# Performance work log

Measured on AMD Instinct MI355X. Metric: run time of the kernel, lower is better.

## Reference

```python
import jax, jax.numpy as jnp
import numpy as np

WS = 16      # window_size
FW = 1       # focal_window -> 3x3 grid of focal windows
FF = 2       # focal_factor (avg-pool for non-center windows)
NH = 8       # num_heads

_OFFSETS = [(di, dj) for di in range(-FW, FW + 1) for dj in range(-FW, FW + 1)]
# tokens contributed by each focal window (center keeps full res, neighbors pooled)
_COUNTS = np.array([WS * WS if (di == 0 and dj == 0) else (WS // FF) ** 2 for di, dj in _OFFSETS])
# center window gets zero bias, peripheral windows get -position_bias (intent of add_focal_bias)
_MULTS = np.array([0.0 if (di == 0 and dj == 0) else -1.0 for di, dj in _OFFSETS], dtype=np.float32)


def _gather_focal(x):
    """x: (B,H,W,C) -> (B*nW, kv_len, C) focal key/value tokens per window."""
    B, H, W, C = x.shape
    nH, nWg = H // WS, W // WS
    xp = jnp.pad(x, ((0, 0), (WS, WS), (WS, WS), (0, 0)), mode='reflect')
    # padded window grid: (B, nH+2, nWg+2, WS, WS, C)
    g = xp.reshape(B, nH + 2, WS, nWg + 2, WS, C).transpose(0, 1, 3, 2, 4, 5)
    parts = []
    for di, dj in _OFFSETS:
        w = g[:, 1 + di:1 + di + nH, 1 + dj:1 + dj + nWg]  # (B,nH,nWg,WS,WS,C)
        if di == 0 and dj == 0:
            t = w.reshape(B, nH, nWg, WS * WS, C)
        else:
            p = WS // FF  # avg_pool2d(kernel=stride=FF)
            t = w.reshape(B, nH, nWg, p, FF, p, FF, C).mean(axis=(4, 6)).reshape(B, nH, nWg, p * p, C)
        parts.append(t)
    kv = jnp.concatenate(parts, axis=3)  # (B,nH,nWg,kv_len,C)
    return kv.reshape(B * nH * nWg, -1, C)


def _bias_tokens(position_bias):
    # (NH, 9) -> (NH, kv_len): per-focal-window bias broadcast over its tokens
    scaled = position_bias * jnp.asarray(_MULTS)[None, :]
    return jnp.repeat(scaled, _COUNTS, axis=1)


def reference(x, Wq, bq, Wk, bk, Wv, bv, Wo, bo, position_bias):
    B, H, W, C = x.shape
    hd = C // NH
    scale = hd ** -0.5
    nH, nWg = H // WS, W // WS
    # window partition: (B*nW, WS*WS, C)
    xw = x.reshape(B, nH, WS, nWg, WS, C).transpose(0, 1, 3, 2, 4, 5).reshape(-1, WS * WS, C)
    kv = _gather_focal(x)  # (B*nW, kv_len, C)
    q = (xw @ Wq + bq).reshape(-1, WS * WS, NH, hd).transpose(0, 2, 1, 3)
    k = (kv @ Wk + bk).reshape(kv.shape[0], -1, NH, hd).transpose(0, 2, 1, 3)
    v = (kv @ Wv + bv).reshape(kv.shape[0], -1, NH, hd).transpose(0, 2, 1, 3)
    attn = jnp.einsum('whqd,whkd->whqk', q, k) * scale
    attn = attn + _bias_tokens(position_bias)[None, :, None, :]
    attn = jax.nn.softmax(attn, axis=-1)
    out = jnp.einsum('whqk,whkd->whqd', attn, v).transpose(0, 2, 1, 3).reshape(-1, WS * WS, C)
    out = out @ Wo + bo
    # window reverse
    out = out.reshape(B, nH, nWg, WS, WS, C).transpose(0, 1, 3, 2, 4, 5).reshape(B, H, W, C)
    return out


def setup_inputs() -> dict:
    key = jax.random.key(0)
    ks = jax.random.split(key, 10)
    D = 384
    w = lambda k: jax.random.normal(k, (D, D), dtype=jnp.float32) * 0.02
    b = lambda k: jax.random.normal(k, (D,), dtype=jnp.float32) * 0.02
    return {
        'x': jax.random.normal(ks[0], (2, 128, 128, D), dtype=jnp.float32),
        'Wq': w(ks[1]), 'bq': b(ks[2]),
        'Wk': w(ks[3]), 'bk': b(ks[4]),
        'Wv': w(ks[5]), 'bv': b(ks[6]),
        'Wo': w(ks[7]), 'bo': b(ks[8]),
        'position_bias': jax.random.normal(ks[9], (NH, 9), dtype=jnp.float32) * 0.02,
    }
```

## Files before the change

kernel.cpp:

```cpp
#include <hip/hip_runtime.h>
#include <hip/hip_bf16.h>

#define NTOK 32768
#define LOG2E 1.4426950408889634f

typedef __attribute__((ext_vector_type(8))) short bf16x8;
typedef __attribute__((ext_vector_type(4))) float f32x4;

__device__ __forceinline__ float bf2f(unsigned short u) {
  return __uint_as_float(((unsigned int)u) << 16);
}
__device__ __forceinline__ unsigned short f2bf(float f) {
  union { __hip_bfloat16 h; unsigned short u; } cv;
  cv.h = __float2bfloat16(f);
  return cv.u;
}
__device__ __forceinline__ float fast_exp2(float x) {
#if __has_builtin(__builtin_amdgcn_exp2f)
  return __builtin_amdgcn_exp2f(x);
#else
  return exp2f(x);
#endif
}

__device__ __forceinline__ void gload16(const void* g, void* l) {
  __builtin_amdgcn_global_load_lds(
      (const __attribute__((address_space(1))) unsigned int*)(unsigned long long)g,
      (__attribute__((address_space(3))) unsigned int*)(unsigned long long)l, 16, 0, 0);
}

__global__ __launch_bounds__(256) void convert_x(const float* __restrict__ x,
                                                 unsigned short* __restrict__ xb) {
  const int i = (blockIdx.x * 256 + threadIdx.x) * 8;
  float4 a = *(const float4*)(x + i);
  float4 b = *(const float4*)(x + i + 4);
  *(ushort4*)(xb + i)     = make_ushort4(f2bf(a.x), f2bf(a.y), f2bf(a.z), f2bf(a.w));
  *(ushort4*)(xb + i + 4) = make_ushort4(f2bf(b.x), f2bf(b.y), f2bf(b.z), f2bf(b.w));
}

__global__ __launch_bounds__(256) void transpose_w(const float* __restrict__ Wq,
                                                   const float* __restrict__ Wk,
                                                   const float* __restrict__ Wv,
                                                   const float* __restrict__ Wo,
                                                   unsigned short* __restrict__ Wt) {
  __shared__ float tile[32][33];
  const int wsel = blockIdx.z;
  const float* W = (wsel == 0) ? Wq : (wsel == 1) ? Wk : (wsel == 2) ? Wv : Wo;
  unsigned short* out = Wt + (size_t)wsel * 147456;
  const int k0 = blockIdx.x * 32, n0 = blockIdx.y * 32;
  const int r = threadIdx.x >> 3, c4 = (threadIdx.x & 7) * 4;
  float4 v = *(const float4*)&W[(size_t)(k0 + r) * 384 + n0 + c4];
  tile[r][c4 + 0] = v.x; tile[r][c4 + 1] = v.y; tile[r][c4 + 2] = v.z; tile[r][c4 + 3] = v.w;
  __syncthreads();
  ushort4 o = make_ushort4(f2bf(tile[c4 + 0][r]), f2bf(tile[c4 + 1][r]),
                           f2bf(tile[c4 + 2][r]), f2bf(tile[c4 + 3][r]));
  *(ushort4*)&out[(size_t)(n0 + r) * 384 + k0 + c4] = o;
}

__global__ __launch_bounds__(128) void pool_kernel(const unsigned short* __restrict__ xb,
                                                   unsigned short* __restrict__ P) {
  int blk = blockIdx.x;
  int b = blk / 6400;
  int rem = blk - b * 6400;
  int p0 = rem / 80, p1 = rem - p0 * 80;
  int i0 = 2 * p0 - 16, i1 = i0 + 1;
  int j0 = 2 * p1 - 16, j1 = j0 + 1;
  int r0 = i0 < 0 ? -i0 : (i0 > 127 ? 254 - i0 : i0);
  int r1 = i1 < 0 ? -i1 : (i1 > 127 ? 254 - i1 : i1);
  int c0 = j0 < 0 ? -j0 : (j0 > 127 ? 254 - j0 : j0);
  int c1 = j1 < 0 ? -j1 : (j1 > 127 ? 254 - j1 : j1);
  const unsigned short* s00 = xb + (((size_t)b * 128 + r0) * 128 + c0) * 384;
  const unsigned short* s01 = xb + (((size_t)b * 128 + r0) * 128 + c1) * 384;
  const unsigned short* s10 = xb + (((size_t)b * 128 + r1) * 128 + c0) * 384;
  const unsigned short* s11 = xb + (((size_t)b * 128 + r1) * 128 + c1) * 384;
  unsigned short* dst = P + (size_t)blk * 384;
  for (int c = threadIdx.x; c < 384; c += 128)
    dst[c] = f2bf(0.25f * (bf2f(s00[c]) + bf2f(s01[c]) + bf2f(s10[c]) + bf2f(s11[c])));
}

__global__ __launch_bounds__(256) void mfma_proj_fused(
    const unsigned short* __restrict__ xb, const unsigned short* __restrict__ P,
    const unsigned short* __restrict__ Wt,
    const float* __restrict__ bq, const float* __restrict__ bk, const float* __restrict__ bv,
    unsigned short* __restrict__ Qb, unsigned short* __restrict__ Kcat,
    unsigned short* __restrict__ Vcat) {
  const int xx = blockIdx.x, yy = blockIdx.y;
  const unsigned short* X;
  int wsel; size_t off;
  if (xx < 9) { X = xb; wsel = xx / 3; off = 0; }
  else { if (yy >= 100) return; X = P; wsel = 1 + (xx - 9) / 3; off = (size_t)NTOK * 384; }
  const float* bias = (wsel == 0) ? bq : (wsel == 1) ? bk : bv;
  unsigned short* Y = ((wsel == 0) ? Qb : (wsel == 1) ? Kcat : Vcat) + off;
  const unsigned short* Wm = Wt + (size_t)wsel * 147456;
  const int n0 = ((xx < 9) ? (xx % 3) : ((xx - 9) % 3)) * 128;
  const int m0 = yy * 128;

  __shared__ __attribute__((aligned(16))) unsigned short As[128 * 32];
  __shared__ __attribute__((aligned(16))) unsigned short Bs[128 * 32];
  const int t = threadIdx.x;
  const int w = t >> 6, l = t & 63, l15 = l & 15, g = l >> 4;
  const int wm = w >> 1, wn = w & 1;

  f32x4 acc[4][4];
  #pragma unroll
  for (int i = 0; i < 4; ++i)
    #pragma unroll
    for (int j = 0; j < 4; ++j) acc[i][j] = {0.f, 0.f, 0.f, 0.f};

  for (int k0 = 0; k0 < 384; k0 += 32) {
    __syncthreads();
    #pragma unroll
    for (int a = 0; a < 2; ++a) {
      const int c = w * 2 + a;
      const int row = c * 16 + (l >> 2), kc = (l & 3) * 8;
      gload16(X  + (size_t)(m0 + row) * 384 + k0 + kc, As + c * 512);
      gload16(Wm + (size_t)(n0 + row) * 384 + k0 + kc, Bs + c * 512);
    }
    __syncthreads();
    bf16x8 af[4], bfr[4];
    #pragma unroll
    for (int mi = 0; mi < 4; ++mi)
      af[mi] = *(const bf16x8*)(As + (wm * 64 + mi * 16 + l15) * 32 + g * 8);
    #pragma unroll
    for (int nj = 0; nj < 4; ++nj)
      bfr[nj] = *(const bf16x8*)(Bs + (wn * 64 + nj * 16 + l15) * 32 + g * 8);
    #pragma unroll
    for (int mi = 0; mi < 4; ++mi)
      #pragma unroll
      for (int nj = 0; nj < 4; ++nj)
        acc[mi][nj] = __builtin_amdgcn_mfma_f32_16x16x32_bf16(af[mi], bfr[nj], acc[mi][nj], 0, 0, 0);
  }

  float bv4[4];
  #pragma unroll
  for (int nj = 0; nj < 4; ++nj) bv4[nj] = bias[n0 + wn * 64 + nj * 16 + l15];
  #pragma unroll
  for (int mi = 0; mi < 4; ++mi)
    #pragma unroll
    for (int nj = 0; nj < 4; ++nj)
      #pragma unroll
      for (int r = 0; r < 4; ++r) {
        const size_t row = m0 + wm * 64 + mi * 16 + g * 4 + r;
        const size_t col = n0 + wn * 64 + nj * 16 + l15;
        Y[row * 384 + col] = f2bf(acc[mi][nj][r] + bv4[nj]);
      }
}

__global__ __launch_bounds__(256) void mfma_proj_out(const unsigned short* __restrict__ X,
                                                     const unsigned short* __restrict__ Wm,
                                                     const float* __restrict__ bias,
                                                     float* __restrict__ Y) {
  const int n0 = blockIdx.x * 128, m0 = blockIdx.y * 128;
  __shared__ __attribute__((aligned(16))) unsigned short As[128 * 32];
  __shared__ __attribute__((aligned(16))) unsigned short Bs[128 * 32];
  const int t = threadIdx.x;
  const int w = t >> 6, l = t & 63, l15 = l & 15, g = l >> 4;
  const int wm = w >> 1, wn = w & 1;

  f32x4 acc[4][4];
  #pragma unroll
  for (int i = 0; i < 4; ++i)
    #pragma unroll
    for (int j = 0; j < 4; ++j) acc[i][j] = {0.f, 0.f, 0.f, 0.f};

  for (int k0 = 0; k0 < 384; k0 += 32) {
    __syncthreads();
    #pragma unroll
    for (int a = 0; a < 2; ++a) {
      const int c = w * 2 + a;
      const int row = c * 16 + (l >> 2), kc = (l & 3) * 8;
      gload16(X  + (size_t)(m0 + row) * 384 + k0 + kc, As + c * 512);
      gload16(Wm + (size_t)(n0 + row) * 384 + k0 + kc, Bs + c * 512);
    }
    __syncthreads();
    bf16x8 af[4], bfr[4];
    #pragma unroll
    for (int mi = 0; mi < 4; ++mi)
      af[mi] = *(const bf16x8*)(As + (wm * 64 + mi * 16 + l15) * 32 + g * 8);
    #pragma unroll
    for (int nj = 0; nj < 4; ++nj)
      bfr[nj] = *(const bf16x8*)(Bs + (wn * 64 + nj * 16 + l15) * 32 + g * 8);
    #pragma unroll
    for (int mi = 0; mi < 4; ++mi)
      #pragma unroll
      for (int nj = 0; nj < 4; ++nj)
        acc[mi][nj] = __builtin_amdgcn_mfma_f32_16x16x32_bf16(af[mi], bfr[nj], acc[mi][nj], 0, 0, 0);
  }

  float bv4[4];
  #pragma unroll
  for (int nj = 0; nj < 4; ++nj) bv4[nj] = bias[n0 + wn * 64 + nj * 16 + l15];
  #pragma unroll
  for (int mi = 0; mi < 4; ++mi)
    #pragma unroll
    for (int nj = 0; nj < 4; ++nj)
      #pragma unroll
      for (int r = 0; r < 4; ++r) {
        const size_t row = m0 + wm * 64 + mi * 16 + g * 4 + r;
        const size_t col = n0 + wn * 64 + nj * 16 + l15;
        Y[row * 384 + col] = acc[mi][nj][r] + bv4[nj];
      }
}

__global__ __launch_bounds__(256) void attn_mfma(const unsigned short* __restrict__ Qg,
                                                 const unsigned short* __restrict__ Kc,
                                                 const unsigned short* __restrict__ Vc,
                                                 const float* __restrict__ pb,
                                                 unsigned short* __restrict__ AttO) {
  __shared__ int kvbase[768];
  __shared__ float tb2s[12];
  __shared__ __attribute__((aligned(16))) unsigned short Ks[2][3072];
  __shared__ __attribute__((aligned(16))) unsigned short Vt[2][64 * 68];
  __shared__ __attribute__((aligned(16))) unsigned short Ps[4][64 * 36];

  const int t = threadIdx.x;
  const int head = blockIdx.x >> 7, win = blockIdx.x & 127;
  const int b = win >> 6, wrem = win & 63, wi = wrem >> 3, wj = wrem & 7;
  const int w = t >> 6, l = t & 63, l15 = l & 15, g = l >> 4;

  for (int j = t; j < 768; j += 256) {
    int o, within;
    if (j < 256)      { o = j >> 6;               within = j & 63; }
    else if (j < 512) { o = 4;                    within = j - 256; }
    else              { o = 5 + ((j - 512) >> 6); within = j & 63; }
    int base;
    if (o == 4) {
      int r = within >> 4, c = within & 15;
      base = ((b * 128 + wi * 16 + r) * 128 + wj * 16 + c) * 384;
    } else {
      int di = o / 3 - 1, dj = o - (o / 3) * 3 - 1;
      int t0 = within >> 3, t1 = within & 7;
      int p0 = 8 * (1 + di + wi) + t0, p1 = 8 * (1 + dj + wj) + t1;
      base = (NTOK + (b * 80 + p0) * 80 + p1) * 384;
    }
    kvbase[j] = base + head * 48;
  }
  if (t < 12) {
    int o = (t < 4) ? t : ((t < 8) ? 4 : t - 3);
    tb2s[t] = (o == 4) ? 0.0f : (-pb[head * 9 + o] * LOG2E);
  }
  for (int idx = t; idx < 2 * 16 * 68; idx += 256) {
    const int bu = idx / 1088, rem = idx - bu * 1088;
    const int rr = rem / 68, cc = rem - rr * 68;
    Vt[bu][(48 + rr) * 68 + cc] = (rr == 0) ? 0x3F80 : 0;
  }

  const float SCALE2 = 0.14433756729740643f * LOG2E;
  const bf16x8 z8 = {0, 0, 0, 0, 0, 0, 0, 0};

  bf16x8 qf[4][2];
  #pragma unroll
  for (int nf = 0; nf < 4; ++nf) {
    const int tok = ((b * 128 + wi * 16 + w * 4 + nf) * 128 + wj * 16 + l15);
    const unsigned short* qp = Qg + (size_t)tok * 384 + head * 48;
    qf[nf][0] = *(const bf16x8*)(qp + g * 8);
    qf[nf][1] = (g < 2) ? *(const bf16x8*)(qp + 32 + g * 8) : z8;
  }

  f32x4 Oacc[4][4];
  #pragma unroll
  for (int mo = 0; mo < 4; ++mo)
    #pragma unroll
    for (int nf = 0; nf < 4; ++nf) Oacc[mo][nf] = {0.f, 0.f, 0.f, 0.f};

  __syncthreads();

  {
    const int kvb = kvbase[l];
    gload16(Kc + kvb + w * 8, &Ks[0][w * 512]);
    if (w < 2) gload16(Kc + kvb + (4 + w) * 8, &Ks[0][(4 + w) * 512]);
  }
  uint4 va0, va1;
  {
    const int kvb = kvbase[l];
    va0 = *(const uint4*)(Vc + kvb + w * 8);
    va1 = (w < 2) ? *(const uint4*)(Vc + kvb + (4 + w) * 8) : make_uint4(0, 0, 0, 0);
  }

  for (int T = 0; T < 12; ++T) {
    const int buf = T & 1;
    asm volatile("s_waitcnt vmcnt(0)" ::: "memory");
    {
      const unsigned short* u0 = (const unsigned short*)&va0;
      #pragma unroll
      for (int s = 0; s < 8; ++s) Vt[buf][(w * 8 + s) * 68 + l] = u0[s];
      if (w < 2) {
        const unsigned short* u1 = (const unsigned short*)&va1;
        #pragma unroll
        for (int s = 0; s < 8; ++s) Vt[buf][((4 + w) * 8 + s) * 68 + l] = u1[s];
      }
    }
    __syncthreads();
    if (T < 11) {
      const int kvb2 = kvbase[(T + 1) * 64 + l];
      gload16(Kc + kvb2 + w * 8, &Ks[buf ^ 1][w * 512]);
      if (w < 2) gload16(Kc + kvb2 + (4 + w) * 8, &Ks[buf ^ 1][(4 + w) * 512]);
      va0 = *(const uint4*)(Vc + kvb2 + w * 8);
      if (w < 2) va1 = *(const uint4*)(Vc + kvb2 + (4 + w) * 8);
    }

    const float tb = tb2s[T];
    #pragma unroll
    for (int h = 0; h < 2; ++h) {
      bf16x8 ka[2][2];
      #pragma unroll
      for (int mi = 0; mi < 2; ++mi) {
        const int krow = h * 32 + mi * 16 + l15;
        ka[mi][0] = *(const bf16x8*)&Ks[buf][g * 512 + krow * 8];
        ka[mi][1] = (g < 2) ? *(const bf16x8*)&Ks[buf][(4 + g) * 512 + krow * 8] : z8;
      }
      #pragma unroll
      for (int nf = 0; nf < 4; ++nf) {
        f32x4 sf0 = {0.f, 0.f, 0.f, 0.f}, sf1 = {0.f, 0.f, 0.f, 0.f};
        sf0 = __builtin_amdgcn_mfma_f32_16x16x32_bf16(ka[0][0], qf[nf][0], sf0, 0, 0, 0);
        sf0 = __builtin_amdgcn_mfma_f32_16x16x32_bf16(ka[0][1], qf[nf][1], sf0, 0, 0, 0);
        sf1 = __builtin_amdgcn_mfma_f32_16x16x32_bf16(ka[1][0], qf[nf][0], sf1, 0, 0, 0);
        sf1 = __builtin_amdgcn_mfma_f32_16x16x32_bf16(ka[1][1], qf[nf][1], sf1, 0, 0, 0);
        float p[8];
        #pragma unroll
        for (int r = 0; r < 4; ++r) {
          p[r]     = fast_exp2(fmaf(sf0[r], SCALE2, tb));
          p[4 + r] = fast_exp2(fmaf(sf1[r], SCALE2, tb));
        }
        #pragma unroll
        for (int mi = 0; mi < 2; ++mi) {
          ushort4 pk = make_ushort4(f2bf(p[mi * 4 + 0]), f2bf(p[mi * 4 + 1]),
                                    f2bf(p[mi * 4 + 2]), f2bf(p[mi * 4 + 3]));
          const int chunk = mi * 2 + (g >> 1);
          *(ushort4*)&Ps[w][(nf * 16 + l15) * 36 + ((chunk ^ (l15 & 3)) << 3) + ((g & 1) << 2)] = pk;
        }
      }
      bf16x8 pbf[4];
      #pragma unroll
      for (int nf = 0; nf < 4; ++nf) {
        const unsigned short* pp = &Ps[w][(nf * 16 + l15) * 36 + ((g ^ (l15 & 3)) << 3)];
        union { bf16x8 v; ushort4 u[2]; } cv;
        cv.u[0] = *(const ushort4*)pp;
        cv.u[1] = *(const ushort4*)(pp + 4);
        pbf[nf] = cv.v;
      }
      #pragma unroll
      for (int mo = 0; mo < 4; ++mo) {
        const unsigned short* vp = &Vt[buf][(mo * 16 + l15) * 68 + h * 32 + g * 8];
        union { bf16x8 v; ushort4 u[2]; } cv;
        cv.u[0] = *(const ushort4*)vp;
        cv.u[1] = *(const ushort4*)(vp + 4);
        bf16x8 va = cv.v;
        #pragma unroll
        for (int nf = 0; nf < 4; ++nf)
          Oacc[mo][nf] = __builtin_amdgcn_mfma_f32_16x16x32_bf16(va, pbf[nf], Oacc[mo][nf], 0, 0, 0);
      }
    }
  }

  #pragma unroll
  for (int nf = 0; nf < 4; ++nf) {
    const float denom = __shfl(Oacc[3][nf][0], l15, 64);
    const float inv = 1.0f / denom;
    const int tok = ((b * 128 + wi * 16 + w * 4 + nf) * 128 + wj * 16 + l15);
    unsigned short* op = AttO + (size_t)tok * 384 + head * 48;
    #pragma unroll
    for (int mo = 0; mo < 3; ++mo) {
      ushort4 u = make_ushort4(f2bf(Oacc[mo][nf][0] * inv), f2bf(Oacc[mo][nf][1] * inv),
                               f2bf(Oacc[mo][nf][2] * inv), f2bf(Oacc[mo][nf][3] * inv));
      *(ushort4*)(op + mo * 16 + g * 4) = u;
    }
  }
}

extern "C" void kernel_launch(void* const* d_in, const int* in_sizes, int n_in,
                              void* d_out, int out_size, void* d_ws, size_t ws_size,
                              hipStream_t stream) {
  const float* x  = (const float*)d_in[0];
  const float* Wq = (const float*)d_in[1];
  const float* bq = (const float*)d_in[2];
  const float* Wk = (const float*)d_in[3];
  const float* bk = (const float*)d_in[4];
  const float* Wv = (const float*)d_in[5];
  const float* bv = (const float*)d_in[6];
  const float* Wo = (const float*)d_in[7];
  const float* bo = (const float*)d_in[8];
  const float* pb = (const float*)d_in[9];

  char* ws = (char*)d_ws;
  unsigned short* Wt   = (unsigned short*)(ws);
  unsigned short* P    = (unsigned short*)(ws + 1179648ull);
  unsigned short* Kcat = (unsigned short*)(ws + 11010048ull);
  unsigned short* Vcat = (unsigned short*)(ws + 46006272ull);
  unsigned short* xb   = (unsigned short*)(ws + 81002496ull);
  unsigned short* AttO = xb;
  unsigned short* Qb   = (unsigned short*)d_out;

  convert_x<<<6144, 256, 0, stream>>>(x, xb);
  pool_kernel<<<12800, 128, 0, stream>>>(xb, P);
  transpose_w<<<dim3(12, 12, 4), 256, 0, stream>>>(Wq, Wk, Wv, Wo, Wt);
  mfma_proj_fused<<<dim3(15, 256), 256, 0, stream>>>(xb, P, Wt, bq, bk, bv, Qb, Kcat, Vcat);
  attn_mfma<<<1024, 256, 0, stream>>>(Qb, Kcat, Vcat, pb, AttO);
  mfma_proj_out<<<dim3(3, 256), 256, 0, stream>>>(AttO, Wt + 3 * 147456, bo, (float*)d_out);
}
```

Baseline: 202.2 us.

## Replace LDS round-trip for P with permlane swaps and flatten projection grid

In the attention kernel the softmax probabilities are now repacked into MFMA operand layout with v_permlane32/16 swap instructions instead of being written to and read back from a per-wave shared-memory buffer, which removes that LDS traffic and frees the LDS space. The QK MFMAs are grouped into one batch and MFMA sections are wrapped in s_setprio, and the kernel gets a launch bound of 4 blocks per SM. The fused projection launch becomes a 1D grid of 2904 blocks, so the early-exiting blocks for the pooled rows are no longer launched. The lane permutation must match the old LDS swizzle exactly, and grouping the score accumulators raises register pressure.

```diff
diff --git a/kernel.cpp b/kernel.cpp
--- a/kernel.cpp
+++ b/kernel.cpp
@@ -14,6 +14,9 @@
   union { __hip_bfloat16 h; unsigned short u; } cv;
   cv.h = __float2bfloat16(f);
   return cv.u;
+}
+__device__ __forceinline__ unsigned pack2(float lo, float hi) {
+  return (unsigned)f2bf(lo) | ((unsigned)f2bf(hi) << 16);
 }
 __device__ __forceinline__ float fast_exp2(float x) {
 #if __has_builtin(__builtin_amdgcn_exp2f)
@@ -84,15 +87,20 @@
     const float* __restrict__ bq, const float* __restrict__ bk, const float* __restrict__ bv,
     unsigned short* __restrict__ Qb, unsigned short* __restrict__ Kcat,
     unsigned short* __restrict__ Vcat) {
-  const int xx = blockIdx.x, yy = blockIdx.y;
+  const int bid = blockIdx.x;
   const unsigned short* X;
-  int wsel; size_t off;
-  if (xx < 9) { X = xb; wsel = xx / 3; off = 0; }
-  else { if (yy >= 100) return; X = P; wsel = 1 + (xx - 9) / 3; off = (size_t)NTOK * 384; }
+  int wsel, colblk, yy; size_t off;
+  if (bid < 2304) {
+    const int xx = bid % 9; yy = bid / 9;
+    X = xb; wsel = xx / 3; colblk = xx % 3; off = 0;
+  } else {
+    const int r = bid - 2304; const int xx = r % 6; yy = r / 6;
+    X = P; wsel = 1 + xx / 3; colblk = xx % 3; off = (size_t)NTOK * 384;
+  }
   const float* bias = (wsel == 0) ? bq : (wsel == 1) ? bk : bv;
   unsigned short* Y = ((wsel == 0) ? Qb : (wsel == 1) ? Kcat : Vcat) + off;
   const unsigned short* Wm = Wt + (size_t)wsel * 147456;
-  const int n0 = ((xx < 9) ? (xx % 3) : ((xx - 9) % 3)) * 128;
+  const int n0 = colblk * 128;
   const int m0 = yy * 128;
 
   __shared__ __attribute__((aligned(16))) unsigned short As[128 * 32];
@@ -202,16 +210,15 @@
       }
 }
 
-__global__ __launch_bounds__(256) void attn_mfma(const unsigned short* __restrict__ Qg,
-                                                 const unsigned short* __restrict__ Kc,
-                                                 const unsigned short* __restrict__ Vc,
-                                                 const float* __restrict__ pb,
-                                                 unsigned short* __restrict__ AttO) {
+__global__ __launch_bounds__(256, 4) void attn_mfma(const unsigned short* __restrict__ Qg,
+                                                    const unsigned short* __restrict__ Kc,
+                                                    const unsigned short* __restrict__ Vc,
+                                                    const float* __restrict__ pb,
+                                                    unsigned short* __restrict__ AttO) {
   __shared__ int kvbase[768];
   __shared__ float tb2s[12];
   __shared__ __attribute__((aligned(16))) unsigned short Ks[2][3072];
   __shared__ __attribute__((aligned(16))) unsigned short Vt[2][64 * 68];
-  __shared__ __attribute__((aligned(16))) unsigned short Ps[4][64 * 36];
 
   const int t = threadIdx.x;
   const int head = blockIdx.x >> 7, win = blockIdx.x & 127;
@@ -309,36 +316,43 @@
         ka[mi][0] = *(const bf16x8*)&Ks[buf][g * 512 + krow * 8];
         ka[mi][1] = (g < 2) ? *(const bf16x8*)&Ks[buf][(4 + g) * 512 + krow * 8] : z8;
       }
+      f32x4 sf[2][4];
+      #pragma unroll
+      for (int mi = 0; mi < 2; ++mi)
+        #pragma unroll
+        for (int nf = 0; nf < 4; ++nf) sf[mi][nf] = {0.f, 0.f, 0.f, 0.f};
+      __builtin_amdgcn_s_setprio(1);
+      #pragma unroll
+      for (int mi = 0; mi < 2; ++mi)
+        #pragma unroll
+        for (int nf = 0; nf < 4; ++nf) {
+          sf[mi][nf] = __builtin_amdgcn_mfma_f32_16x16x32_bf16(ka[mi][0], qf[nf][0], sf[mi][nf], 0, 0, 0);
+          sf[mi][nf] = __builtin_amdgcn_mfma_f32_16x16x32_bf16(ka[mi][1], qf[nf][1], sf[mi][nf], 0, 0, 0);
+        }
+      __builtin_amdgcn_s_setprio(0);
+
+      bf16x8 pbf[4];
       #pragma unroll
       for (int nf = 0; nf < 4; ++nf) {
-        f32x4 sf0 = {0.f, 0.f, 0.f, 0.f}, sf1 = {0.f, 0.f, 0.f, 0.f};
-        sf0 = __builtin_amdgcn_mfma_f32_16x16x32_bf16(ka[0][0], qf[nf][0], sf0, 0, 0, 0);
-        sf0 = __builtin_amdgcn_mfma_f32_16x16x32_bf16(ka[0][1], qf[nf][1], sf0, 0, 0, 0);
-        sf1 = __builtin_amdgcn_mfma_f32_16x16x32_bf16(ka[1][0], qf[nf][0], sf1, 0, 0, 0);
-        sf1 = __builtin_amdgcn_mfma_f32_16x16x32_bf16(ka[1][1], qf[nf][1], sf1, 0, 0, 0);
         float p[8];
         #pragma unroll
         for (int r = 0; r < 4; ++r) {
-          p[r]     = fast_exp2(fmaf(sf0[r], SCALE2, tb));
-          p[4 + r] = fast_exp2(fmaf(sf1[r], SCALE2, tb));
+          p[r]     = fast_exp2(fmaf(sf[0][nf][r], SCALE2, tb));
+          p[4 + r] = fast_exp2(fmaf(sf[1][nf][r], SCALE2, tb));
         }
-        #pragma unroll
-        for (int mi = 0; mi < 2; ++mi) {
-          ushort4 pk = make_ushort4(f2bf(p[mi * 4 + 0]), f2bf(p[mi * 4 + 1]),
-                                    f2bf(p[mi * 4 + 2]), f2bf(p[mi * 4 + 3]));
-          const int chunk = mi * 2 + (g >> 1);
-          *(ushort4*)&Ps[w][(nf * 16 + l15) * 36 + ((chunk ^ (l15 & 3)) << 3) + ((g & 1) << 2)] = pk;
-        }
-      }
-      bf16x8 pbf[4];
-      #pragma unroll
-      for (int nf = 0; nf < 4; ++nf) {
-        const unsigned short* pp = &Ps[w][(nf * 16 + l15) * 36 + ((g ^ (l15 & 3)) << 3)];
-        union { bf16x8 v; ushort4 u[2]; } cv;
-        cv.u[0] = *(const ushort4*)pp;
-        cv.u[1] = *(const ushort4*)(pp + 4);
+        unsigned a0 = pack2(p[0], p[1]);
+        unsigned a1 = pack2(p[2], p[3]);
+        unsigned b0 = pack2(p[4], p[5]);
+        unsigned b1 = pack2(p[6], p[7]);
+        asm("v_permlane32_swap_b32 %0, %1" : "+v"(a0), "+v"(b0));
+        asm("v_permlane32_swap_b32 %0, %1" : "+v"(a1), "+v"(b1));
+        asm("v_permlane16_swap_b32 %0, %1" : "+v"(a0), "+v"(b0));
+        asm("v_permlane16_swap_b32 %0, %1" : "+v"(a1), "+v"(b1));
+        union { bf16x8 v; unsigned u[4]; } cv;
+        cv.u[0] = a0; cv.u[1] = a1; cv.u[2] = b0; cv.u[3] = b1;
         pbf[nf] = cv.v;
       }
+
       #pragma unroll
       for (int mo = 0; mo < 4; ++mo) {
         const unsigned short* vp = &Vt[buf][(mo * 16 + l15) * 68 + h * 32 + g * 8];
@@ -346,9 +360,11 @@
         cv.u[0] = *(const ushort4*)vp;
         cv.u[1] = *(const ushort4*)(vp + 4);
         bf16x8 va = cv.v;
+        __builtin_amdgcn_s_setprio(1);
         #pragma unroll
         for (int nf = 0; nf < 4; ++nf)
           Oacc[mo][nf] = __builtin_amdgcn_mfma_f32_16x16x32_bf16(va, pbf[nf], Oacc[mo][nf], 0, 0, 0);
+        __builtin_amdgcn_s_setprio(0);
       }
     }
   }
@@ -394,7 +410,7 @@
   convert_x<<<6144, 256, 0, stream>>>(x, xb);
   pool_kernel<<<12800, 128, 0, stream>>>(xb, P);
   transpose_w<<<dim3(12, 12, 4), 256, 0, stream>>>(Wq, Wk, Wv, Wo, Wt);
-  mfma_proj_fused<<<dim3(15, 256), 256, 0, stream>>>(xb, P, Wt, bq, bk, bv, Qb, Kcat, Vcat);
+  mfma_proj_fused<<<2904, 256, 0, stream>>>(xb, P, Wt, bq, bk, bv, Qb, Kcat, Vcat);
   attn_mfma<<<1024, 256, 0, stream>>>(Qb, Kcat, Vcat, pb, AttO);
   mfma_proj_out<<<dim3(3, 256), 256, 0, stream>>>(AttO, Wt + 3 * 147456, bo, (float*)d_out);
 }
```

Measured after the change: 343.5 us. +69.9%, slower.
